# Performance work log

Hardware: AMD Instinct MI355X
Metric: run time of the kernel (lower is better)

Reference implementation:

```python
import jax, jax.numpy as jnp
import numpy as np

DIM = 1024

def setup_inputs() -> dict:
    key = jax.random.key(0)
    ks = jax.random.split(key, 7)
    s = 1.0 / np.sqrt(DIM)
    x = jax.random.normal(ks[0], (8, 2048, DIM), dtype=jnp.float32)
    Wq = jax.random.uniform(ks[1], (DIM, DIM), jnp.float32, -s, s)
    bq = jax.random.uniform(ks[2], (DIM,), jnp.float32, -s, s)
    Wk = jax.random.uniform(ks[3], (DIM, DIM), jnp.float32, -s, s)
    bk = jax.random.uniform(ks[4], (DIM,), jnp.float32, -s, s)
    Wv = jax.random.uniform(ks[5], (DIM, DIM), jnp.float32, -s, s)
    bv = jax.random.uniform(ks[6], (DIM,), jnp.float32, -s, s)
    return {"x": x, "Wq": Wq, "bq": bq, "Wk": Wk, "bk": bk, "Wv": Wv, "bv": bv}

def reference(x, Wq, bq, Wk, bk, Wv, bv):
    # nn.Linear: y = x @ W.T + b
    q = jnp.einsum('bsd,ed->bse', x, Wq) + bq  # [B,S,D]
    k = jnp.einsum('bsd,ed->bse', x, Wk) + bk
    v = jnp.einsum('bsd,ed->bse', x, Wv) + bv
    scores = jnp.einsum('bqd,bkd->bqk', q, k) / jnp.sqrt(jnp.float32(DIM))
    attn = jax.nn.softmax(scores, axis=-1)
    return jnp.einsum('bqk,bkd->bqd', attn, v)
```

## Files before the change

kernel.cpp:

```cpp
#include <hip/hip_runtime.h>

#define DIM 1024
#define SEQ 2048

typedef __attribute__((ext_vector_type(8))) short bf16x8;
typedef __attribute__((ext_vector_type(16))) float f32x16;
typedef __attribute__((ext_vector_type(4))) unsigned short us4;
typedef __attribute__((ext_vector_type(4))) _Float16 h4;

__device__ __forceinline__ unsigned short f2bf(float f) {
    union { float f; unsigned int u; } v; v.f = f;
    unsigned int r = (v.u + 0x7FFFu + ((v.u >> 16) & 1u)) >> 16;
    return (unsigned short)r;
}

#define GLOAD(gp, lp) __builtin_amdgcn_global_load_lds( \
    (const __attribute__((address_space(1))) unsigned int*)(gp), \
    (__attribute__((address_space(3))) unsigned int*)(lp), 16, 0, 0)

#define MFMA32(a, b, c) __builtin_amdgcn_mfma_f32_32x32x16_bf16((a), (b), (c), 0, 0, 0)

__global__ __launch_bounds__(256) void cast_f32_bf16(const float* __restrict__ src,
                                                     unsigned short* __restrict__ dst, int n) {
    int i = (blockIdx.x * 256 + threadIdx.x) * 8;
    if (i >= n) return;
    float4 a = *(const float4*)(src + i);
    float4 b = *(const float4*)(src + i + 4);
    us4 lo = { f2bf(a.x), f2bf(a.y), f2bf(a.z), f2bf(a.w) };
    us4 hi = { f2bf(b.x), f2bf(b.y), f2bf(b.z), f2bf(b.w) };
    *(us4*)(dst + i) = lo;
    *(us4*)(dst + i + 4) = hi;
}

__device__ __forceinline__ void gemm256_core(
    const unsigned short* __restrict__ A, const unsigned short* __restrict__ B,
    int lda, int ldb, int K, char* smem, f32x16 acc[4][2])
{
    const int tid = threadIdx.x;
    const int lane = tid & 63;
    const int wm = (tid >> 6) >> 2;
    const int wn = (tid >> 6) & 3;
    const int l31 = lane & 31, lhi = lane >> 5;

    const int schunk = ((tid & 7) ^ ((tid >> 3) & 7)) * 8;
    const unsigned short* paw = A + (size_t)(tid >> 3) * lda + schunk;
    const unsigned short* pbw = B + (size_t)(tid >> 3) * ldb + schunk;
    const int doff = tid * 16;

    const int key = l31 & 7;
    const int abase = (wm * 128 + l31) * 128;
    const int bbase = 32768 + (wn * 64 + l31) * 128;
    int csw[4];
#pragma unroll
    for (int ks = 0; ks < 4; ks++) csw[ks] = (((ks << 1) | lhi) ^ key) * 16;

    const int NT = K >> 6;

#define STAGE_A(bb, kt) do { \
    GLOAD(paw + (kt),                       smem + (bb) + doff); \
    GLOAD(paw + (kt) + (size_t)64  * lda,   smem + (bb) + 8192 + doff); \
    GLOAD(paw + (kt) + (size_t)128 * lda,   smem + (bb) + 16384 + doff); \
    GLOAD(paw + (kt) + (size_t)192 * lda,   smem + (bb) + 24576 + doff); \
} while (0)
#define STAGE_B(bb, kt) do { \
    GLOAD(pbw + (kt),                       smem + (bb) + 32768 + doff); \
    GLOAD(pbw + (kt) + (size_t)64  * ldb,   smem + (bb) + 40960 + doff); \
    GLOAD(pbw + (kt) + (size_t)128 * ldb,   smem + (bb) + 49152 + doff); \
    GLOAD(pbw + (kt) + (size_t)192 * ldb,   smem + (bb) + 57344 + doff); \
} while (0)

    STAGE_A(0, 0);
    STAGE_B(0, 0);

    for (int T = 0; T < NT; ++T) {
        asm volatile("s_waitcnt vmcnt(0)" ::: "memory");
        __builtin_amdgcn_s_barrier();
        const char* db = smem + (T & 1) * 65536;
        const int nb = ((T + 1) & 1) * 65536;
        bf16x8 a0[4], a1[4], b0[2], b1[2];

#pragma unroll
        for (int mi = 0; mi < 4; mi++) {
            a0[mi] = *(const bf16x8*)(db + abase + mi * 4096 + csw[0]);
            a1[mi] = *(const bf16x8*)(db + abase + mi * 4096 + csw[1]);
        }
#pragma unroll
        for (int nj = 0; nj < 2; nj++) {
            b0[nj] = *(const bf16x8*)(db + bbase + nj * 4096 + csw[0]);
            b1[nj] = *(const bf16x8*)(db + bbase + nj * 4096 + csw[1]);
        }
        if (T + 1 < NT) STAGE_A(nb, (size_t)(T + 1) * 64);
        __builtin_amdgcn_s_setprio(1);
#pragma unroll
        for (int mi = 0; mi < 4; mi++)
#pragma unroll
            for (int nj = 0; nj < 2; nj++)
                acc[mi][nj] = MFMA32(a0[mi], b0[nj], acc[mi][nj]);
#pragma unroll
        for (int mi = 0; mi < 4; mi++)
#pragma unroll
            for (int nj = 0; nj < 2; nj++)
                acc[mi][nj] = MFMA32(a1[mi], b1[nj], acc[mi][nj]);
        __builtin_amdgcn_s_setprio(0);

#pragma unroll
        for (int mi = 0; mi < 4; mi++) {
            a0[mi] = *(const bf16x8*)(db + abase + mi * 4096 + csw[2]);
            a1[mi] = *(const bf16x8*)(db + abase + mi * 4096 + csw[3]);
        }
#pragma unroll
        for (int nj = 0; nj < 2; nj++) {
            b0[nj] = *(const bf16x8*)(db + bbase + nj * 4096 + csw[2]);
            b1[nj] = *(const bf16x8*)(db + bbase + nj * 4096 + csw[3]);
        }
        if (T + 1 < NT) STAGE_B(nb, (size_t)(T + 1) * 64);
        __builtin_amdgcn_s_setprio(1);
#pragma unroll
        for (int mi = 0; mi < 4; mi++)
#pragma unroll
            for (int nj = 0; nj < 2; nj++)
                acc[mi][nj] = MFMA32(a0[mi], b0[nj], acc[mi][nj]);
#pragma unroll
        for (int mi = 0; mi < 4; mi++)
#pragma unroll
            for (int nj = 0; nj < 2; nj++)
                acc[mi][nj] = MFMA32(a1[mi], b1[nj], acc[mi][nj]);
        __builtin_amdgcn_s_setprio(0);
    }
#undef STAGE_A
#undef STAGE_B
}

#define ACC_INIT() \
    f32x16 acc[4][2]; \
    _Pragma("unroll") for (int i = 0; i < 4; i++) \
    _Pragma("unroll") for (int jj = 0; jj < 2; jj++) acc[i][jj] = (f32x16){}; \


template<int BZ>
__global__ __launch_bounds__(512, 2) void gemm_qkv_t(
    const unsigned short* __restrict__ xb, const unsigned short* __restrict__ w,
    const float* __restrict__ bias, unsigned short* __restrict__ C)
{
    extern __shared__ char smem[];
    const int bid = blockIdx.x;
    const int lb = (bid & 7) * 32 + (bid >> 3);
    const int m0 = (lb >> 2) * 256, n0 = (lb & 3) * 256;
    ACC_INIT();
    gemm256_core(xb + (size_t)m0 * DIM, w + (size_t)n0 * DIM, DIM, DIM, DIM, smem, acc);
    const int lane = threadIdx.x & 63, wid = threadIdx.x >> 6;
    const int wm = wid >> 2, wn = wid & 3;
    const int l31 = lane & 31, lhi = lane >> 5;
    const float scale = (BZ == 0) ? 0.03125f : 1.0f;
#pragma unroll
    for (int mi = 0; mi < 4; mi++)
#pragma unroll
        for (int nj = 0; nj < 2; nj++) {
            const int col = n0 + wn * 64 + nj * 32 + l31;
            const float bcol = bias[col];
            if (BZ < 2) {
#pragma unroll
                for (int r = 0; r < 16; r++) {
                    const int row = m0 + wm * 128 + mi * 32 + (r & 3) + 8 * (r >> 2) + 4 * lhi;
                    C[(size_t)row * DIM + col] = f2bf((acc[mi][nj][r] + bcol) * scale);
                }
            } else {
#pragma unroll
                for (int r4 = 0; r4 < 4; r4++) {
                    const int s0 = m0 + wm * 128 + mi * 32 + 8 * r4 + 4 * lhi;
                    const int b = s0 >> 11, s = s0 & 2047;
                    us4 pk = { f2bf(acc[mi][nj][r4 * 4] + bcol),
                               f2bf(acc[mi][nj][r4 * 4 + 1] + bcol),
                               f2bf(acc[mi][nj][r4 * 4 + 2] + bcol),
                               f2bf(acc[mi][nj][r4 * 4 + 3] + bcol) };
                    *(us4*)&C[((size_t)b << 21) + ((size_t)col << 11) + s] = pk;
                }
            }
        }
}

__global__ __launch_bounds__(512, 2) void gemm_qk(
    const unsigned short* __restrict__ qb, const unsigned short* __restrict__ kb,
    unsigned short* __restrict__ sb)
{
    extern __shared__ char smem[];
    const int bid = blockIdx.x;
    const int lb = (bid & 7) * 64 + (bid >> 3);
    const int b = lb >> 6;
    const int r0 = lb & 63;
    const int m0 = (r0 >> 3) * 256, n0 = (r0 & 7) * 256;
    ACC_INIT();
    gemm256_core(qb + ((size_t)b * SEQ + m0) * DIM, kb + ((size_t)b * SEQ + n0) * DIM,
                 DIM, DIM, DIM, smem, acc);
    const int lane = threadIdx.x & 63, wid = threadIdx.x >> 6;
    const int wm = wid >> 2, wn = wid & 3;
    const int l31 = lane & 31, lhi = lane >> 5;
    _Float16* sh = (_Float16*)sb + (size_t)b * SEQ * SEQ;
#pragma unroll
    for (int mi = 0; mi < 4; mi++)
#pragma unroll
        for (int nj = 0; nj < 2; nj++) {
            const int col = n0 + wn * 64 + nj * 32 + l31;
#pragma unroll
            for (int r = 0; r < 16; r++) {
                const int row = m0 + wm * 128 + mi * 32 + (r & 3) + 8 * (r >> 2) + 4 * lhi;
                sh[(size_t)row * SEQ + col] = (_Float16)acc[mi][nj][r];
            }
        }
}

__global__ __launch_bounds__(256) void softmax_p(unsigned short* __restrict__ sb)
{
    const int lane = threadIdx.x & 63, wid = threadIdx.x >> 6;
    const size_t row = (size_t)blockIdx.x * 4 + wid;
    unsigned short* rp = sb + row * SEQ;
    float v[32];
#pragma unroll
    for (int j = 0; j < 8; j++) {
        h4 h = *(const h4*)(rp + (j * 64 + lane) * 4);
#pragma unroll
        for (int e = 0; e < 4; e++) v[j * 4 + e] = (float)h[e];
    }
    float m = -1e30f;
#pragma unroll
    for (int i = 0; i < 32; i++) m = fmaxf(m, v[i]);
#pragma unroll
    for (int msk = 1; msk <= 32; msk <<= 1) m = fmaxf(m, __shfl_xor(m, msk, 64));
    float s = 0.f;
#pragma unroll
    for (int i = 0; i < 32; i++) { v[i] = __expf(v[i] - m); s += v[i]; }
#pragma unroll
    for (int msk = 1; msk <= 32; msk <<= 1) s += __shfl_xor(s, msk, 64);
    float inv = 1.0f / s;
#pragma unroll
    for (int j = 0; j < 8; j++) {
        us4 pu = { f2bf(v[j * 4] * inv), f2bf(v[j * 4 + 1] * inv),
                   f2bf(v[j * 4 + 2] * inv), f2bf(v[j * 4 + 3] * inv) };
        *(us4*)(rp + (j * 64 + lane) * 4) = pu;
    }
}

__global__ __launch_bounds__(512, 2) void gemm_pv(
    const unsigned short* __restrict__ pb, const unsigned short* __restrict__ vt,
    float* __restrict__ out)
{
    extern __shared__ char smem[];
    const int bid = blockIdx.x;
    const int lb = (bid & 7) * 32 + (bid >> 3);
    const int b = lb >> 5;
    const int r0 = lb & 31;
    const int m0 = (r0 >> 2) * 256, n0 = (r0 & 3) * 256;
    ACC_INIT();
    gemm256_core(pb + ((size_t)b * SEQ + m0) * SEQ, vt + ((size_t)b * DIM + n0) * SEQ,
                 SEQ, SEQ, SEQ, smem, acc);
    const int lane = threadIdx.x & 63, wid = threadIdx.x >> 6;
    const int wm = wid >> 2, wn = wid & 3;
    const int l31 = lane & 31, lhi = lane >> 5;
    float* O = out + (size_t)b * SEQ * DIM;
#pragma unroll
    for (int mi = 0; mi < 4; mi++)
#pragma unroll
        for (int nj = 0; nj < 2; nj++) {
            const int col = n0 + wn * 64 + nj * 32 + l31;
#pragma unroll
            for (int r = 0; r < 16; r++) {
                const int row = m0 + wm * 128 + mi * 32 + (r & 3) + 8 * (r >> 2) + 4 * lhi;
                O[(size_t)row * DIM + col] = acc[mi][nj][r];
            }
        }
}

extern "C" void kernel_launch(void* const* d_in, const int* in_sizes, int n_in,
                              void* d_out, int out_size, void* d_ws, size_t ws_size,
                              hipStream_t stream) {
    const float* x  = (const float*)d_in[0];
    const float* Wq = (const float*)d_in[1];
    const float* bq = (const float*)d_in[2];
    const float* Wk = (const float*)d_in[3];
    const float* bk = (const float*)d_in[4];
    const float* Wv = (const float*)d_in[5];
    const float* bv = (const float*)d_in[6];
    float* out = (float*)d_out;
    char* ws = (char*)d_ws;

    unsigned short* xb = (unsigned short*)(ws);
    unsigned short* wb = (unsigned short*)(ws + 33554432);
    unsigned short* qb = (unsigned short*)(ws + 39845888);
    unsigned short* kb = (unsigned short*)(ws + 73400320);
    unsigned short* vt = (unsigned short*)(ws + 106954752);
    unsigned short* sb = (unsigned short*)(ws + 140509184);

    cast_f32_bf16<<<dim3(8192), 256, 0, stream>>>(x, xb, 16777216);
    cast_f32_bf16<<<dim3(512), 256, 0, stream>>>(Wq, wb, 1048576);
    cast_f32_bf16<<<dim3(512), 256, 0, stream>>>(Wk, wb + 1048576, 1048576);
    cast_f32_bf16<<<dim3(512), 256, 0, stream>>>(Wv, wb + 2097152, 1048576);

    hipFuncSetAttribute((const void*)gemm_qkv_t<0>, hipFuncAttributeMaxDynamicSharedMemorySize, 131072);
    hipFuncSetAttribute((const void*)gemm_qkv_t<1>, hipFuncAttributeMaxDynamicSharedMemorySize, 131072);
    hipFuncSetAttribute((const void*)gemm_qkv_t<2>, hipFuncAttributeMaxDynamicSharedMemorySize, 131072);
    hipFuncSetAttribute((const void*)gemm_qk,  hipFuncAttributeMaxDynamicSharedMemorySize, 131072);
    hipFuncSetAttribute((const void*)gemm_pv,  hipFuncAttributeMaxDynamicSharedMemorySize, 131072);

    gemm_qkv_t<0><<<dim3(256), 512, 131072, stream>>>(xb, wb,           bq, qb);
    gemm_qkv_t<1><<<dim3(256), 512, 131072, stream>>>(xb, wb + 1048576, bk, kb);
    gemm_qkv_t<2><<<dim3(256), 512, 131072, stream>>>(xb, wb + 2097152, bv, vt);
    gemm_qk<<<dim3(512), 512, 131072, stream>>>(qb, kb, sb);
    softmax_p<<<dim3(4096), 256, 0, stream>>>(sb);
    gemm_pv<<<dim3(256), 512, 131072, stream>>>(sb, vt, out);
}
```

Measured before the change: 286.8 us.

## Restructure GEMM main loop into four-phase ping-pong schedule with staggered prefetch

Rewrites the 256x256 bf16 GEMM mainloop into four sub-phases, each covering one quadrant of the per-wave tile (two M blocks by one N block). Global-to-LDS loads are split into half-tiles and interleaved between phases, and B is prefetched two iterations ahead into the buffer being read. Barriers and lgkmcnt/vmcnt waits are placed so waves alternate between LDS reads and MFMA bursts. The aim is to hide load latency and reduce the single full vmcnt(0) stall per iteration, at the cost of many more barriers per iteration and a more fragile buffer-reuse ordering.

```diff
diff --git a/kernel.cpp b/kernel.cpp
--- a/kernel.cpp
+++ b/kernel.cpp
@@ -56,79 +56,99 @@
 
     const int NT = K >> 6;
 
-#define STAGE_A(bb, kt) do { \
-    GLOAD(paw + (kt),                       smem + (bb) + doff); \
-    GLOAD(paw + (kt) + (size_t)64  * lda,   smem + (bb) + 8192 + doff); \
-    GLOAD(paw + (kt) + (size_t)128 * lda,   smem + (bb) + 16384 + doff); \
-    GLOAD(paw + (kt) + (size_t)192 * lda,   smem + (bb) + 24576 + doff); \
+#define SA(dbb, kt, h) do { \
+    GLOAD(paw + (kt) + (size_t)((h) * 128)      * lda, smem + (dbb) + (h) * 16384 + doff); \
+    GLOAD(paw + (kt) + (size_t)((h) * 128 + 64) * lda, smem + (dbb) + (h) * 16384 + 8192 + doff); \
 } while (0)
-#define STAGE_B(bb, kt) do { \
-    GLOAD(pbw + (kt),                       smem + (bb) + 32768 + doff); \
-    GLOAD(pbw + (kt) + (size_t)64  * ldb,   smem + (bb) + 40960 + doff); \
-    GLOAD(pbw + (kt) + (size_t)128 * ldb,   smem + (bb) + 49152 + doff); \
-    GLOAD(pbw + (kt) + (size_t)192 * ldb,   smem + (bb) + 57344 + doff); \
+#define SB(dbb, kt, h) do { \
+    GLOAD(pbw + (kt) + (size_t)((h) * 128)      * ldb, smem + (dbb) + 32768 + (h) * 16384 + doff); \
+    GLOAD(pbw + (kt) + (size_t)((h) * 128 + 64) * ldb, smem + (dbb) + 32768 + (h) * 16384 + 8192 + doff); \
 } while (0)
 
-    STAGE_A(0, 0);
-    STAGE_B(0, 0);
+    SA(0, 0, 0); SA(0, 0, 1);
+    SB(0, 0, 0); SB(0, 0, 1);
+    SB(65536, 64, 0); SB(65536, 64, 1);
+    asm volatile("s_waitcnt vmcnt(4)" ::: "memory");
+    __builtin_amdgcn_s_barrier();
+
+    bf16x8 a[8], b0[4], b1[4];
 
     for (int T = 0; T < NT; ++T) {
-        asm volatile("s_waitcnt vmcnt(0)" ::: "memory");
-        __builtin_amdgcn_s_barrier();
         const char* db = smem + (T & 1) * 65536;
-        const int nb = ((T + 1) & 1) * 65536;
-        bf16x8 a0[4], a1[4], b0[2], b1[2];
-
-#pragma unroll
-        for (int mi = 0; mi < 4; mi++) {
-            a0[mi] = *(const bf16x8*)(db + abase + mi * 4096 + csw[0]);
-            a1[mi] = *(const bf16x8*)(db + abase + mi * 4096 + csw[1]);
-        }
-#pragma unroll
-        for (int nj = 0; nj < 2; nj++) {
-            b0[nj] = *(const bf16x8*)(db + bbase + nj * 4096 + csw[0]);
-            b1[nj] = *(const bf16x8*)(db + bbase + nj * 4096 + csw[1]);
-        }
-        if (T + 1 < NT) STAGE_A(nb, (size_t)(T + 1) * 64);
+        const int nd = ((T + 1) & 1) * 65536;
+        const int sd = (T & 1) * 65536;
+
+#pragma unroll
+        for (int mi = 0; mi < 2; mi++)
+#pragma unroll
+            for (int ks = 0; ks < 4; ks++)
+                a[mi * 4 + ks] = *(const bf16x8*)(db + abase + mi * 4096 + csw[ks]);
+#pragma unroll
+        for (int ks = 0; ks < 4; ks++)
+            b0[ks] = *(const bf16x8*)(db + bbase + csw[ks]);
+        if (T + 1 < NT) SA(nd, (size_t)(T + 1) * 64, 0);
+        asm volatile("s_waitcnt lgkmcnt(8)" ::: "memory");
+        __builtin_amdgcn_s_barrier();
+        asm volatile("s_waitcnt lgkmcnt(0)" ::: "memory");
+        __builtin_amdgcn_sched_barrier(0);
         __builtin_amdgcn_s_setprio(1);
 #pragma unroll
-        for (int mi = 0; mi < 4; mi++)
-#pragma unroll
-            for (int nj = 0; nj < 2; nj++)
-                acc[mi][nj] = MFMA32(a0[mi], b0[nj], acc[mi][nj]);
-#pragma unroll
-        for (int mi = 0; mi < 4; mi++)
-#pragma unroll
-            for (int nj = 0; nj < 2; nj++)
-                acc[mi][nj] = MFMA32(a1[mi], b1[nj], acc[mi][nj]);
+        for (int ks = 0; ks < 4; ks++)
+#pragma unroll
+            for (int mi = 0; mi < 2; mi++)
+                acc[mi][0] = MFMA32(a[mi * 4 + ks], b0[ks], acc[mi][0]);
         __builtin_amdgcn_s_setprio(0);
-
-#pragma unroll
-        for (int mi = 0; mi < 4; mi++) {
-            a0[mi] = *(const bf16x8*)(db + abase + mi * 4096 + csw[2]);
-            a1[mi] = *(const bf16x8*)(db + abase + mi * 4096 + csw[3]);
-        }
-#pragma unroll
-        for (int nj = 0; nj < 2; nj++) {
-            b0[nj] = *(const bf16x8*)(db + bbase + nj * 4096 + csw[2]);
-            b1[nj] = *(const bf16x8*)(db + bbase + nj * 4096 + csw[3]);
-        }
-        if (T + 1 < NT) STAGE_B(nb, (size_t)(T + 1) * 64);
+        __builtin_amdgcn_s_barrier();
+
+#pragma unroll
+        for (int ks = 0; ks < 4; ks++)
+            b1[ks] = *(const bf16x8*)(db + bbase + 4096 + csw[ks]);
+        if (T + 1 < NT) SA(nd, (size_t)(T + 1) * 64, 1);
+        __builtin_amdgcn_s_barrier();
+        asm volatile("s_waitcnt lgkmcnt(0)" ::: "memory");
+        __builtin_amdgcn_sched_barrier(0);
         __builtin_amdgcn_s_setprio(1);
 #pragma unroll
-        for (int mi = 0; mi < 4; mi++)
-#pragma unroll
-            for (int nj = 0; nj < 2; nj++)
-                acc[mi][nj] = MFMA32(a0[mi], b0[nj], acc[mi][nj]);
-#pragma unroll
-        for (int mi = 0; mi < 4; mi++)
-#pragma unroll
-            for (int nj = 0; nj < 2; nj++)
-                acc[mi][nj] = MFMA32(a1[mi], b1[nj], acc[mi][nj]);
+        for (int ks = 0; ks < 4; ks++)
+#pragma unroll
+            for (int mi = 0; mi < 2; mi++)
+                acc[mi][1] = MFMA32(a[mi * 4 + ks], b1[ks], acc[mi][1]);
         __builtin_amdgcn_s_setprio(0);
+        __builtin_amdgcn_s_barrier();
+
+#pragma unroll
+        for (int mi = 0; mi < 2; mi++)
+#pragma unroll
+            for (int ks = 0; ks < 4; ks++)
+                a[mi * 4 + ks] = *(const bf16x8*)(db + abase + (mi + 2) * 4096 + csw[ks]);
+        if (T + 2 < NT) SB(sd, (size_t)(T + 2) * 64, 0);
+        __builtin_amdgcn_s_barrier();
+        asm volatile("s_waitcnt lgkmcnt(0)" ::: "memory");
+        __builtin_amdgcn_sched_barrier(0);
+        __builtin_amdgcn_s_setprio(1);
+#pragma unroll
+        for (int ks = 0; ks < 4; ks++)
+#pragma unroll
+            for (int mi = 0; mi < 2; mi++)
+                acc[mi + 2][0] = MFMA32(a[mi * 4 + ks], b0[ks], acc[mi + 2][0]);
+        __builtin_amdgcn_s_setprio(0);
+        __builtin_amdgcn_s_barrier();
+
+        if (T + 2 < NT) SB(sd, (size_t)(T + 2) * 64, 1);
+        __builtin_amdgcn_s_barrier();
+        __builtin_amdgcn_s_setprio(1);
+#pragma unroll
+        for (int ks = 0; ks < 4; ks++)
+#pragma unroll
+            for (int mi = 0; mi < 2; mi++)
+                acc[mi + 2][1] = MFMA32(a[mi * 4 + ks], b1[ks], acc[mi + 2][1]);
+        __builtin_amdgcn_s_setprio(0);
+        if (T + 2 < NT) asm volatile("s_waitcnt vmcnt(4)" ::: "memory");
+        else            asm volatile("s_waitcnt vmcnt(0)" ::: "memory");
+        __builtin_amdgcn_s_barrier();
     }
-#undef STAGE_A
-#undef STAGE_B
+#undef SA
+#undef SB
 }
 
 #define ACC_INIT() \
@@ -151,7 +171,6 @@
     const int lane = threadIdx.x & 63, wid = threadIdx.x >> 6;
     const int wm = wid >> 2, wn = wid & 3;
     const int l31 = lane & 31, lhi = lane >> 5;
-    const float scale = (BZ == 0) ? 0.03125f : 1.0f;
 #pragma unroll
     for (int mi = 0; mi < 4; mi++)
 #pragma unroll
@@ -159,6 +178,7 @@
             const int col = n0 + wn * 64 + nj * 32 + l31;
             const float bcol = bias[col];
             if (BZ < 2) {
+                const float scale = (BZ == 0) ? 0.03125f : 1.0f;
 #pragma unroll
                 for (int r = 0; r < 16; r++) {
                     const int row = m0 + wm * 128 + mi * 32 + (r & 3) + 8 * (r >> 2) + 4 * lhi;
```

Result: slower. 317.1 us (+10.6%).
